# Performance work log

Hardware: AMD Instinct MI355X
Metric: run time of the kernel (lower is better)

The kernel has to match this reference:

```python
import jax, jax.numpy as jnp
import numpy as np

HEADS = 8
HEAD_DIM = 32
SCALE = HEAD_DIM ** (-0.5)


def setup_inputs() -> dict:
    key = jax.random.key(0)
    k1, k2, k3 = jax.random.split(key, 3)
    B, DIM, N = 4, 512, 2048
    INNER = HEADS * HEAD_DIM  # 256
    x = jax.random.normal(k1, (B, DIM, N), dtype=jnp.float32)
    # Conv1d(kernel=1, bias=False) == channel-mixing matmul; weight (out_ch, in_ch)
    w_qkv = jax.random.normal(k2, (3 * INNER, DIM), dtype=jnp.float32) * (DIM ** -0.5)
    w_out = jax.random.normal(k3, (DIM, INNER), dtype=jnp.float32) * (INNER ** -0.5)
    b_out = jnp.zeros((DIM,), dtype=jnp.float32)
    return {"x": x, "w_qkv": w_qkv, "w_out": w_out, "b_out": b_out}


def reference(x, w_qkv, w_out, b_out):
    B, DIM, N = x.shape
    INNER = HEADS * HEAD_DIM
    # to_qkv: 1x1 conv over channels, then permute(0,2,1) -> (B, N, 3*INNER)
    qkv = jnp.einsum('bcn,oc->bno', x, w_qkv)
    q, k, v = jnp.split(qkv, 3, axis=-1)
    # 'b n (h d) -> b h n d'
    def to_heads(t):
        return t.reshape(B, N, HEADS, HEAD_DIM).transpose(0, 2, 1, 3)
    q, k, v = to_heads(q), to_heads(k), to_heads(v)
    # L2 similarity: -||q_i - k_j||_2 * scale, via expansion (avoids O(N^2 d) tensor)
    q2 = jnp.sum(q * q, axis=-1)            # (B,H,N)
    k2 = jnp.sum(k * k, axis=-1)            # (B,H,N)
    qk = jnp.einsum('bhid,bhjd->bhij', q, k)  # (B,H,N,N)
    dist2 = q2[..., :, None] + k2[..., None, :] - 2.0 * qk
    smi = -jnp.sqrt(jnp.maximum(dist2, 1e-12)) * SCALE
    attn = jax.nn.softmax(smi, axis=-1)
    out = jnp.einsum('bhij,bhjd->bhid', attn, v)  # (B,H,N,d)
    # 'b h n d -> b (h d) n'
    out = out.transpose(0, 1, 3, 2).reshape(B, INNER, N)
    # to_out: 1x1 conv with bias
    return jnp.einsum('bcn,oc->bon', out, w_out) + b_out[None, :, None]
```

## Files before the change

### kernel.cpp

```cpp
#include <hip/hip_runtime.h>
#include <math.h>

#define N_SEQ 2048
#define DIMC 512
#define INNER 256
#define C2F (0.17677669529663687f * 1.4426950408889634f)
#define C2F2 (C2F * C2F)

typedef short bf16x8 __attribute__((ext_vector_type(8)));
typedef float f32x4 __attribute__((ext_vector_type(4)));


static __device__ __forceinline__ ushort f2bf(float f) {
    uint x = __float_as_uint(f);
    x += 0x7fff + ((x >> 16) & 1);
    return (ushort)(x >> 16);
}
static __device__ __forceinline__ float bf2f(ushort u) {
    return __uint_as_float(((uint)u) << 16);
}
static __device__ __forceinline__ float fast_exp2_neg(float x) {
    float r; asm("v_exp_f32 %0, -%1" : "=v"(r) : "v"(x)); return r;
}
static __device__ __forceinline__ float fast_sqrt(float x) {
    float r; asm("v_sqrt_f32 %0, %1" : "=v"(r) : "v"(x)); return r;
}

__global__ void xpose_cvt(const float* __restrict__ x, ushort* __restrict__ xt) {
    __shared__ __align__(16) ushort T[64][72];
    const int b = blockIdx.z;
    const int c0 = blockIdx.y * 64;
    const int n0 = blockIdx.x * 64;
    const int t = threadIdx.x;
    const int cl = t >> 4;
    const int n4 = (t & 15) * 4;
    const float* xb = x + ((size_t)b * DIMC + c0) * N_SEQ + n0;
#pragma unroll
    for (int cc = 0; cc < 4; ++cc) {
        const int c = cl + cc * 16;
        float4 v = *(const float4*)(xb + (size_t)c * N_SEQ + n4);
        T[n4 + 0][c] = f2bf(v.x);
        T[n4 + 1][c] = f2bf(v.y);
        T[n4 + 2][c] = f2bf(v.z);
        T[n4 + 3][c] = f2bf(v.w);
    }
    __syncthreads();
    const int nl = t >> 2;
    const int c16 = (t & 3) * 16;
    uint4 v0 = *(const uint4*)&T[nl][c16];
    uint4 v1 = *(const uint4*)&T[nl][c16 + 8];
    ushort* dst = xt + ((size_t)b * N_SEQ + n0 + nl) * DIMC + c0 + c16;
    *(uint4*)dst = v0;
    *(uint4*)(dst + 8) = v1;
}

__global__ void wcvt2(const float* __restrict__ wq, const float* __restrict__ wo,
                      ushort* __restrict__ wq16, ushort* __restrict__ wo16) {
    const int bid = blockIdx.x;
    if (bid < 384) {
        int i = (bid * 256 + threadIdx.x) * 4;
        float4 v = *(const float4*)(wq + i);
        ushort4 p;
        p.x = f2bf(v.x); p.y = f2bf(v.y); p.z = f2bf(v.z); p.w = f2bf(v.w);
        *(ushort4*)(wq16 + i) = p;
    } else {
        int i = ((bid - 384) * 256 + threadIdx.x) * 4;
        float4 v = *(const float4*)(wo + i);
        ushort4 p;
        p.x = f2bf(v.x); p.y = f2bf(v.y); p.z = f2bf(v.z); p.w = f2bf(v.w);
        *(ushort4*)(wo16 + i) = p;
    }
}

__global__ __launch_bounds__(256) void qkv_mfma(const ushort* __restrict__ xt,
        const ushort* __restrict__ w16, ushort* __restrict__ ws16) {
    __shared__ __align__(16) ushort Wls[4 * 520];
    __shared__ __align__(16) ushort Xls[4 * 520];
    const int b = blockIdx.z;
    const int o0 = blockIdx.y * 64;
    const int n0 = blockIdx.x * 64;
    const int t = threadIdx.x;
    const int l = t & 63, w = t >> 6;
    const int q15 = l & 15, g = l >> 4;
    f32x4 acc[4];
#pragma unroll
    for (int nn = 0; nn < 4; ++nn) acc[nn] = (f32x4){0.f, 0.f, 0.f, 0.f};
    const int srow = t >> 2, sg = t & 3;
    const ushort* wsrc = w16 + (size_t)(o0 + srow) * DIMC + sg * 8;
    const ushort* xsrc = xt + ((size_t)b * N_SEQ + n0 + srow) * DIMC + sg * 8;
    uint4 wreg = *(const uint4*)wsrc;
    uint4 xreg = *(const uint4*)xsrc;
    for (int k0 = 0; k0 < DIMC; k0 += 32) {
        __builtin_amdgcn_s_barrier();
        __builtin_amdgcn_sched_barrier(0);
        *(uint4*)(Wls + sg * 520 + srow * 8) = wreg;
        *(uint4*)(Xls + sg * 520 + srow * 8) = xreg;
        if (k0 + 32 < DIMC) {
            wreg = *(const uint4*)(wsrc + k0 + 32);
            xreg = *(const uint4*)(xsrc + k0 + 32);
        }
        asm volatile("s_waitcnt lgkmcnt(0)" ::: "memory");
        __builtin_amdgcn_s_barrier();
        __builtin_amdgcn_sched_barrier(0);
        bf16x8 af = *(const bf16x8*)(Wls + g * 520 + (16 * w + q15) * 8);
        __builtin_amdgcn_s_setprio(1);
#pragma unroll
        for (int nn = 0; nn < 4; ++nn) {
            bf16x8 bfr = *(const bf16x8*)(Xls + g * 520 + (16 * nn + q15) * 8);
            acc[nn] = __builtin_amdgcn_mfma_f32_16x16x32_bf16(af, bfr, acc[nn], 0, 0, 0);
        }
        __builtin_amdgcn_s_setprio(0);
    }
    const int oatom = o0 + 16 * w;
    const int t_idx = oatom >> 8;
    const int h = (oatom >> 5) & 7;
    const int bh = b * 8 + h;
    const int d0 = (oatom & 31) + 4 * g;
    if (t_idx < 2) {
        ushort* dst = ws16 + (size_t)t_idx * 2097152 + (size_t)bh * 65536
                      + (size_t)(d0 >> 3) * 16384 + (d0 & 7);
#pragma unroll
        for (int nn = 0; nn < 4; ++nn) {
            const int n_ = n0 + 16 * nn + q15;
            ushort4 p;
            p.x = f2bf(acc[nn][0]); p.y = f2bf(acc[nn][1]);
            p.z = f2bf(acc[nn][2]); p.w = f2bf(acc[nn][3]);
            *(ushort4*)(dst + (size_t)n_ * 8) = p;
        }
    } else {
        ushort* dst = ws16 + (size_t)4194304 + (size_t)bh * 65536;
#pragma unroll
        for (int nn = 0; nn < 4; ++nn) {
            const int n_ = n0 + 16 * nn + q15;
            ushort* dd = dst + (size_t)(n_ >> 3) * 256 + (n_ & 7);
            dd[(d0 + 0) * 8] = f2bf(acc[nn][0]);
            dd[(d0 + 1) * 8] = f2bf(acc[nn][1]);
            dd[(d0 + 2) * 8] = f2bf(acc[nn][2]);
            dd[(d0 + 3) * 8] = f2bf(acc[nn][3]);
        }
    }
}

__global__ void sq_kernel(const ushort* __restrict__ ws16, float* __restrict__ k2) {
    const int idx = blockIdx.x * 256 + threadIdx.x;
    const int bh = idx >> 11, n = idx & 2047;
    const ushort* base = ws16 + 2097152 + (size_t)bh * 65536 + (size_t)n * 8;
    float s = 0.f;
#pragma unroll
    for (int g = 0; g < 4; ++g) {
        uint4 v = *(const uint4*)(base + (size_t)g * 16384);
        uint a[4] = {v.x, v.y, v.z, v.w};
#pragma unroll
        for (int e = 0; e < 4; ++e) {
            float lo = bf2f((ushort)(a[e] & 0xffff));
            float hi = bf2f((ushort)(a[e] >> 16));
            s += lo * lo + hi * hi;
        }
    }
    k2[idx] = s * (float)C2F2;
}

__global__ __launch_bounds__(256, 4) void attn_kernel(
        const ushort* __restrict__ ws16, const float* __restrict__ k2g,
        ushort* __restrict__ att16) {
    __shared__ __align__(16) ushort Pls[4][16][140];
    const int bid = blockIdx.x;
    const int sw = (bid & 7) * 128 + (bid >> 3);
    const int q0 = (sw & 31) * 64;
    const int bh = sw >> 5;
    const int b = bh >> 3, h = bh & 7;
    const int tid = threadIdx.x;
    const int l = tid & 63;
    const int w = tid >> 6;
    const int q15 = l & 15;
    const int g = l >> 4;
    const int qrow = q0 + 16 * w + q15;

    const ushort* Qbh = ws16 + (size_t)bh * 65536;
    const ushort* Kf = ws16 + 2097152 + (size_t)bh * 65536
                       + (size_t)g * 16384 + (size_t)q15 * 8;
    const ushort* Vf = ws16 + 4194304 + (size_t)bh * 65536 + (size_t)q15 * 8;
    const float* k2p = k2g + (size_t)bh * 2048 + 4 * g;

    const bf16x8 qf = *(const bf16x8*)(Qbh + (size_t)g * 16384 + (size_t)qrow * 8);
    float q2l = 0.f;
#pragma unroll
    for (int e = 0; e < 8; ++e) {
        float qe = bf2f((ushort)qf[e]);
        q2l = fmaf(qe, qe, q2l);
    }
    q2l += __shfl_xor(q2l, 16);
    q2l += __shfl_xor(q2l, 32);
    const float q2v = q2l * (float)C2F2;

    ushort* plane = &Pls[w][q15][0];
    f32x4 accO[2];
    accO[0] = (f32x4){0.f, 0.f, 0.f, 0.f};
    accO[1] = (f32x4){0.f, 0.f, 0.f, 0.f};
    float lsm = 0.f;

    f32x4 st[4];
    bf16x8 kf[4];
    float4 kkA[4], kkB[4];

#pragma unroll
    for (int k = 0; k < 4; ++k) kkA[k] = *(const float4*)(k2p + 16 * k);
#pragma unroll
    for (int k = 0; k < 4; ++k) kf[k] = *(const bf16x8*)(Kf + (size_t)(16 * k) * 8);
    {
        const f32x4 zz = (f32x4){0.f, 0.f, 0.f, 0.f};
#pragma unroll
        for (int k = 0; k < 4; ++k)
            st[k] = __builtin_amdgcn_mfma_f32_16x16x32_bf16(kf[k], qf, zz, 0, 0, 0);
    }

#define ATTN_ITER(H, KKC, KKN)                                                  \
    {                                                                           \
        const int jb = (H) * 64;                                                \
        const int hp = (H) & 1;                                                 \
        bf16x8 vfr[4];                                                          \
        _Pragma("unroll")                                                       \
        for (int jc = 0; jc < 2; ++jc) {                                        \
            const int c = 8 * (H) + 4 * jc + g;                                 \
            vfr[jc * 2 + 0] = *(const bf16x8*)(Vf + (size_t)c * 256);           \
            vfr[jc * 2 + 1] = *(const bf16x8*)(Vf + (size_t)c * 256 + 128);     \
        }                                                                       \
        _Pragma("unroll")                                                       \
        for (int k = 0; k < 4; ++k)                                             \
            KKN[k] = *(const float4*)(k2p + jb + 64 + 16 * k);                  \
        _Pragma("unroll")                                                       \
        for (int k = 0; k < 4; ++k)                                             \
            kf[k] = *(const bf16x8*)(Kf + (size_t)(jb + 64 + 16 * k) * 8);      \
        float lt = 0.f;                                                         \
        _Pragma("unroll")                                                       \
        for (int k = 0; k < 4; ++k) {                                           \
            float ka[4] = {KKC[k].x, KKC[k].y, KKC[k].z, KKC[k].w};             \
            float pr[4];                                                        \
            _Pragma("unroll")                                                   \
            for (int r = 0; r < 4; ++r) {                                       \
                float a = q2v + ka[r];                                          \
                float d2 = fmaf(-2.f * (float)C2F2, st[k][r], a);               \
                pr[r] = fast_exp2_neg(fast_sqrt(fmaxf(d2, 1e-12f)));            \
            }                                                                   \
            lt += (pr[0] + pr[1]) + (pr[2] + pr[3]);                            \
            uint pk0, pk1;                                                      \
            asm("v_cvt_pk_bf16_f32 %0, %1, %2" : "=v"(pk0) : "v"(pr[0]), "v"(pr[1])); \
            asm("v_cvt_pk_bf16_f32 %0, %1, %2" : "=v"(pk1) : "v"(pr[2]), "v"(pr[3])); \
            uint2 pv; pv.x = pk0; pv.y = pk1;                                   \
            *(uint2*)(plane + 16 * (4 * hp + k) + 4 * g) = pv;                  \
        }                                                                       \
        lsm += lt;                                                              \
        const f32x4 zz = (f32x4){0.f, 0.f, 0.f, 0.f};                           \
        __builtin_amdgcn_s_setprio(1);                                          \
        _Pragma("unroll")                                                       \
        for (int k = 0; k < 4; ++k)                                             \
            st[k] = __builtin_amdgcn_mfma_f32_16x16x32_bf16(kf[k], qf, zz, 0, 0, 0); \
        __builtin_amdgcn_s_setprio(0);                                          \
        __builtin_amdgcn_s_setprio(1);                                          \
        _Pragma("unroll")                                                       \
        for (int jc = 0; jc < 2; ++jc) {                                        \
            bf16x8 pf = *(const bf16x8*)(plane + 32 * (2 * hp + jc) + 8 * g);   \
            accO[0] = __builtin_amdgcn_mfma_f32_16x16x32_bf16(vfr[jc * 2 + 0], pf, accO[0], 0, 0, 0); \
            accO[1] = __builtin_amdgcn_mfma_f32_16x16x32_bf16(vfr[jc * 2 + 1], pf, accO[1], 0, 0, 0); \
        }                                                                       \
        __builtin_amdgcn_s_setprio(0);                                          \
    }

#pragma unroll 1
    for (int hh = 0; hh < 32; hh += 2) {
        ATTN_ITER(hh, kkA, kkB)
        ATTN_ITER(hh + 1, kkB, kkA)
    }
#undef ATTN_ITER

    lsm += __shfl_xor(lsm, 16);
    lsm += __shfl_xor(lsm, 32);
    const float invl = 1.f / lsm;
    ushort* dst = att16 + ((size_t)(b * N_SEQ + qrow)) * INNER + h * 32 + 4 * g;
#pragma unroll
    for (int d = 0; d < 2; ++d) {
        ushort4 o;
        o.x = f2bf(accO[d][0] * invl); o.y = f2bf(accO[d][1] * invl);
        o.z = f2bf(accO[d][2] * invl); o.w = f2bf(accO[d][3] * invl);
        *(ushort4*)(dst + d * 16) = o;
    }
}

__global__ __launch_bounds__(256) void out_mfma(const ushort* __restrict__ att16,
        const ushort* __restrict__ wo16, const float* __restrict__ bias,
        float* __restrict__ out) {
    __shared__ __align__(16) ushort Wls[4 * 520];
    __shared__ __align__(16) ushort Als[4 * 520];
    const int b = blockIdx.z;
    const int o0 = blockIdx.y * 64;
    const int n0 = blockIdx.x * 64;
    const int t = threadIdx.x;
    const int l = t & 63, w = t >> 6;
    const int q15 = l & 15, g = l >> 4;
    f32x4 acc[4];
#pragma unroll
    for (int nn = 0; nn < 4; ++nn) acc[nn] = (f32x4){0.f, 0.f, 0.f, 0.f};
    const int srow = t >> 2, sg = t & 3;
    const ushort* wsrc = wo16 + (size_t)(o0 + srow) * INNER + sg * 8;
    const ushort* asrc = att16 + ((size_t)b * N_SEQ + n0 + srow) * INNER + sg * 8;
    uint4 wreg = *(const uint4*)wsrc;
    uint4 areg = *(const uint4*)asrc;
    for (int k0 = 0; k0 < INNER; k0 += 32) {
        __builtin_amdgcn_s_barrier();
        __builtin_amdgcn_sched_barrier(0);
        *(uint4*)(Wls + sg * 520 + srow * 8) = wreg;
        *(uint4*)(Als + sg * 520 + srow * 8) = areg;
        if (k0 + 32 < INNER) {
            wreg = *(const uint4*)(wsrc + k0 + 32);
            areg = *(const uint4*)(asrc + k0 + 32);
        }
        asm volatile("s_waitcnt lgkmcnt(0)" ::: "memory");
        __builtin_amdgcn_s_barrier();
        __builtin_amdgcn_sched_barrier(0);
        bf16x8 af = *(const bf16x8*)(Wls + g * 520 + (16 * w + q15) * 8);
        __builtin_amdgcn_s_setprio(1);
#pragma unroll
        for (int nn = 0; nn < 4; ++nn) {
            bf16x8 bfr = *(const bf16x8*)(Als + g * 520 + (16 * nn + q15) * 8);
            acc[nn] = __builtin_amdgcn_mfma_f32_16x16x32_bf16(af, bfr, acc[nn], 0, 0, 0);
        }
        __builtin_amdgcn_s_setprio(0);
    }
    const int obase = o0 + 16 * w + 4 * g;
    float4 bi = *(const float4*)(bias + obase);
    float* ob = out + ((size_t)b * DIMC + obase) * N_SEQ;
#pragma unroll
    for (int nn = 0; nn < 4; ++nn) {
        const int n_ = n0 + 16 * nn + q15;
        ob[0 * N_SEQ + n_] = acc[nn][0] + bi.x;
        ob[1 * N_SEQ + n_] = acc[nn][1] + bi.y;
        ob[2 * N_SEQ + n_] = acc[nn][2] + bi.z;
        ob[3 * N_SEQ + n_] = acc[nn][3] + bi.w;
    }
}

extern "C" void kernel_launch(void* const* d_in, const int* in_sizes, int n_in,
                              void* d_out, int out_size, void* d_ws, size_t ws_size,
                              hipStream_t stream) {
    const float* x = (const float*)d_in[0];
    const float* w_qkv = (const float*)d_in[1];
    const float* w_out = (const float*)d_in[2];
    const float* b_out = (const float*)d_in[3];
    ushort* ws16 = (ushort*)d_ws;
    float* k2f = (float*)((char*)d_ws + (12 << 20) + (256 << 10));
    ushort* att16 = (ushort*)((char*)d_ws + (13 << 20));
    ushort* xt16 = (ushort*)((char*)d_ws + (21 << 20));
    ushort* wq16 = (ushort*)((char*)d_ws + (29 << 20));
    ushort* wo16 = (ushort*)((char*)d_ws + (30 << 20));
    float* out = (float*)d_out;

    xpose_cvt<<<dim3(32, 8, 4), 256, 0, stream>>>(x, xt16);
    wcvt2<<<dim3(512), 256, 0, stream>>>(w_qkv, w_out, wq16, wo16);
    qkv_mfma<<<dim3(32, 12, 4), 256, 0, stream>>>(xt16, wq16, ws16);
    sq_kernel<<<dim3(256), 256, 0, stream>>>(ws16, k2f);
    attn_kernel<<<dim3(1024), 256, 0, stream>>>(ws16, k2f, att16);
    out_mfma<<<dim3(32, 8, 4), 256, 0, stream>>>(att16, wo16, b_out, out);
}
```

Before: 90.76 us.

## Stage K/V tiles and k2 into LDS via async global_load_lds double buffering

Each block previously had every wave read its K, V and k2 fragments straight from global memory in registers, with software pipelining across iterations. The new code has each block cooperatively load 64-key K and V tiles into double-buffered LDS with direct global-to-LDS loads, and preloads all of k2 into LDS once. Waves then read their fragments from LDS, cutting redundant global and L2 traffic across the four waves. The cost is two block barriers per tile, extra LDS (about 24KB) that may lower occupancy, and losing the previous register-level overlap of QK MFMA with the softmax math.

```diff
diff --git a/kernel.cpp b/kernel.cpp
--- a/kernel.cpp
+++ b/kernel.cpp
@@ -24,6 +24,11 @@
 }
 static __device__ __forceinline__ float fast_sqrt(float x) {
     float r; asm("v_sqrt_f32 %0, %1" : "=v"(r) : "v"(x)); return r;
+}
+static __device__ __forceinline__ void gload16(const void* g, void* l) {
+    __builtin_amdgcn_global_load_lds(
+        (const __attribute__((address_space(1))) void*)g,
+        (__attribute__((address_space(3))) void*)l, 16, 0, 0);
 }
 
 __global__ void xpose_cvt(const float* __restrict__ x, ushort* __restrict__ xt) {
@@ -163,7 +168,10 @@
 __global__ __launch_bounds__(256, 4) void attn_kernel(
         const ushort* __restrict__ ws16, const float* __restrict__ k2g,
         ushort* __restrict__ att16) {
-    __shared__ __align__(16) ushort Pls[4][16][140];
+    __shared__ __align__(16) ushort Kls[2 * 2048];
+    __shared__ __align__(16) ushort Vls[2 * 2048];
+    __shared__ __align__(16) float k2ls[2048];
+    __shared__ __align__(16) ushort Pls[4][16][72];
     const int bid = blockIdx.x;
     const int sw = (bid & 7) * 128 + (bid >> 3);
     const int q0 = (sw & 31) * 64;
@@ -177,10 +185,22 @@
     const int qrow = q0 + 16 * w + q15;
 
     const ushort* Qbh = ws16 + (size_t)bh * 65536;
-    const ushort* Kf = ws16 + 2097152 + (size_t)bh * 65536
-                       + (size_t)g * 16384 + (size_t)q15 * 8;
-    const ushort* Vf = ws16 + 4194304 + (size_t)bh * 65536 + (size_t)q15 * 8;
-    const float* k2p = k2g + (size_t)bh * 2048 + 4 * g;
+    const ushort* Kbh = ws16 + 2097152 + (size_t)bh * 65536;
+    const ushort* Vbh = ws16 + 4194304 + (size_t)bh * 65536;
+    const float* k2bh = k2g + (size_t)bh * 2048;
+
+#define STAGE(T, BUF)                                                         \
+    {                                                                         \
+        const int j0s = (T) * 64;                                             \
+        gload16(Kbh + (size_t)w * 16384 + (size_t)(j0s + l) * 8,              \
+                Kls + (BUF) * 2048 + w * 512);                                \
+        gload16(Vbh + (size_t)j0s * 32 + (size_t)w * 512 + (size_t)l * 8,     \
+                Vls + (BUF) * 2048 + w * 512);                                \
+    }
+
+    gload16(k2bh + (size_t)(2 * w + 0) * 256 + (size_t)l * 4, k2ls + (2 * w + 0) * 256);
+    gload16(k2bh + (size_t)(2 * w + 1) * 256 + (size_t)l * 4, k2ls + (2 * w + 1) * 256);
+    STAGE(0, 0)
 
     const bf16x8 qf = *(const bf16x8*)(Qbh + (size_t)g * 16384 + (size_t)qrow * 8);
     float q2l = 0.f;
@@ -199,42 +219,31 @@
     accO[1] = (f32x4){0.f, 0.f, 0.f, 0.f};
     float lsm = 0.f;
 
-    f32x4 st[4];
-    bf16x8 kf[4];
-    float4 kkA[4], kkB[4];
-
-#pragma unroll
-    for (int k = 0; k < 4; ++k) kkA[k] = *(const float4*)(k2p + 16 * k);
-#pragma unroll
-    for (int k = 0; k < 4; ++k) kf[k] = *(const bf16x8*)(Kf + (size_t)(16 * k) * 8);
-    {
-        const f32x4 zz = (f32x4){0.f, 0.f, 0.f, 0.f};
-#pragma unroll
-        for (int k = 0; k < 4; ++k)
-            st[k] = __builtin_amdgcn_mfma_f32_16x16x32_bf16(kf[k], qf, zz, 0, 0, 0);
-    }
-
-#define ATTN_ITER(H, KKC, KKN)                                                  \
+    asm volatile("s_waitcnt vmcnt(0)" ::: "memory");
+    __builtin_amdgcn_s_barrier();
+    __builtin_amdgcn_sched_barrier(0);
+
+#define COMPUTE(T)                                                              \
     {                                                                           \
-        const int jb = (H) * 64;                                                \
-        const int hp = (H) & 1;                                                 \
-        bf16x8 vfr[4];                                                          \
-        _Pragma("unroll")                                                       \
-        for (int jc = 0; jc < 2; ++jc) {                                        \
-            const int c = 8 * (H) + 4 * jc + g;                                 \
-            vfr[jc * 2 + 0] = *(const bf16x8*)(Vf + (size_t)c * 256);           \
-            vfr[jc * 2 + 1] = *(const bf16x8*)(Vf + (size_t)c * 256 + 128);     \
-        }                                                                       \
+        const ushort* KlsP = Kls + ((T) & 1) * 2048;                            \
+        const ushort* VlsP = Vls + ((T) & 1) * 2048;                            \
+        const int jb = (T) * 64;                                                \
+        bf16x8 kf[4];                                                           \
         _Pragma("unroll")                                                       \
         for (int k = 0; k < 4; ++k)                                             \
-            KKN[k] = *(const float4*)(k2p + jb + 64 + 16 * k);                  \
+            kf[k] = *(const bf16x8*)(KlsP + g * 512 + (16 * k + q15) * 8);      \
+        const f32x4 zz = (f32x4){0.f, 0.f, 0.f, 0.f};                           \
+        f32x4 st[4];                                                            \
+        __builtin_amdgcn_s_setprio(1);                                          \
         _Pragma("unroll")                                                       \
         for (int k = 0; k < 4; ++k)                                             \
-            kf[k] = *(const bf16x8*)(Kf + (size_t)(jb + 64 + 16 * k) * 8);      \
+            st[k] = __builtin_amdgcn_mfma_f32_16x16x32_bf16(kf[k], qf, zz, 0, 0, 0); \
+        __builtin_amdgcn_s_setprio(0);                                          \
         float lt = 0.f;                                                         \
         _Pragma("unroll")                                                       \
         for (int k = 0; k < 4; ++k) {                                           \
-            float ka[4] = {KKC[k].x, KKC[k].y, KKC[k].z, KKC[k].w};             \
+            float4 kk = *(const float4*)(k2ls + jb + 16 * k + 4 * g);           \
+            float ka[4] = {kk.x, kk.y, kk.z, kk.w};                             \
             float pr[4];                                                        \
             _Pragma("unroll")                                                   \
             for (int r = 0; r < 4; ++r) {                                       \
@@ -247,31 +256,39 @@
             asm("v_cvt_pk_bf16_f32 %0, %1, %2" : "=v"(pk0) : "v"(pr[0]), "v"(pr[1])); \
             asm("v_cvt_pk_bf16_f32 %0, %1, %2" : "=v"(pk1) : "v"(pr[2]), "v"(pr[3])); \
             uint2 pv; pv.x = pk0; pv.y = pk1;                                   \
-            *(uint2*)(plane + 16 * (4 * hp + k) + 4 * g) = pv;                  \
+            *(uint2*)(plane + 16 * k + 4 * g) = pv;                             \
         }                                                                       \
         lsm += lt;                                                              \
-        const f32x4 zz = (f32x4){0.f, 0.f, 0.f, 0.f};                           \
-        __builtin_amdgcn_s_setprio(1);                                          \
-        _Pragma("unroll")                                                       \
-        for (int k = 0; k < 4; ++k)                                             \
-            st[k] = __builtin_amdgcn_mfma_f32_16x16x32_bf16(kf[k], qf, zz, 0, 0, 0); \
-        __builtin_amdgcn_s_setprio(0);                                          \
         __builtin_amdgcn_s_setprio(1);                                          \
         _Pragma("unroll")                                                       \
         for (int jc = 0; jc < 2; ++jc) {                                        \
-            bf16x8 pf = *(const bf16x8*)(plane + 32 * (2 * hp + jc) + 8 * g);   \
-            accO[0] = __builtin_amdgcn_mfma_f32_16x16x32_bf16(vfr[jc * 2 + 0], pf, accO[0], 0, 0, 0); \
-            accO[1] = __builtin_amdgcn_mfma_f32_16x16x32_bf16(vfr[jc * 2 + 1], pf, accO[1], 0, 0, 0); \
+            bf16x8 pf = *(const bf16x8*)(plane + 32 * jc + 8 * g);              \
+            _Pragma("unroll")                                                   \
+            for (int dh = 0; dh < 2; ++dh) {                                    \
+                bf16x8 vf = *(const bf16x8*)(VlsP + (4 * jc + g) * 256          \
+                                             + (16 * dh + q15) * 8);            \
+                accO[dh] = __builtin_amdgcn_mfma_f32_16x16x32_bf16(vf, pf, accO[dh], 0, 0, 0); \
+            }                                                                   \
         }                                                                       \
         __builtin_amdgcn_s_setprio(0);                                          \
     }
 
 #pragma unroll 1
-    for (int hh = 0; hh < 32; hh += 2) {
-        ATTN_ITER(hh, kkA, kkB)
-        ATTN_ITER(hh + 1, kkB, kkA)
-    }
-#undef ATTN_ITER
+    for (int t = 0; t < 31; ++t) {
+        STAGE(t + 1, (t + 1) & 1)
+        asm volatile("s_waitcnt vmcnt(2)" ::: "memory");
+        __builtin_amdgcn_s_barrier();
+        __builtin_amdgcn_sched_barrier(0);
+        COMPUTE(t)
+        __builtin_amdgcn_sched_barrier(0);
+        __builtin_amdgcn_s_barrier();
+    }
+    asm volatile("s_waitcnt vmcnt(0)" ::: "memory");
+    __builtin_amdgcn_s_barrier();
+    __builtin_amdgcn_sched_barrier(0);
+    COMPUTE(31)
+#undef COMPUTE
+#undef STAGE
 
     lsm += __shfl_xor(lsm, 16);
     lsm += __shfl_xor(lsm, 32);
```

New measurement: 89.06 us. Within noise of the previous version (-1.9%).
